# Optimization experiments

Hardware: AMD Instinct MI355X
Metric: run time of the kernel (lower is better)

Reference implementation:

```python
import jax, jax.numpy as jnp
import numpy as np

B, N, HID = 2, 2048, 1024
NH = 16
HD = HID // NH

def setup_inputs() -> dict:
    key = jax.random.key(0)
    ks = jax.random.split(key, 5)
    s = 0.02
    return {
        "hidden_states": jax.random.normal(ks[0], (B, N, HID), jnp.float32),
        "attention_mask": jnp.zeros((B, 1, 1, N), jnp.float32),
        "Wq": jax.random.normal(ks[1], (HID, HID), jnp.float32) * s,
        "bq": jnp.zeros((HID,), jnp.float32),
        "Wk": jax.random.normal(ks[2], (HID, HID), jnp.float32) * s,
        "bk": jnp.zeros((HID,), jnp.float32),
        "Wv": jax.random.normal(ks[3], (HID, HID), jnp.float32) * s,
        "bv": jnp.zeros((HID,), jnp.float32),
    }

def reference(hidden_states, attention_mask, Wq, bq, Wk, bk, Wv, bv):
    b, n, _ = hidden_states.shape
    def split_heads(t):  # [b,n,hid] -> [b,h,n,d]
        return t.reshape(b, n, NH, HD).transpose(0, 2, 1, 3)
    q = split_heads(hidden_states @ Wq.T + bq)
    k = split_heads(hidden_states @ Wk.T + bk)
    v = split_heads(hidden_states @ Wv.T + bv)
    scores = jnp.einsum('bhnd,bhmd->bhnm', q, k) / jnp.sqrt(jnp.float32(HD)).astype(q.dtype)
    scores = scores + attention_mask
    scores = jnp.maximum(scores, jnp.finfo(scores.dtype).min)
    probs = jax.nn.softmax(scores, axis=-1)
    out = jnp.einsum('bhnm,bhmd->bhnd', probs, v)
    return out.transpose(0, 2, 1, 3).reshape(b, n, NH * HD)
```

## Files before the change

### kernel.cpp

```cpp
#include <hip/hip_runtime.h>

typedef unsigned short u16;
typedef unsigned int   u32;
typedef __attribute__((ext_vector_type(8))) short bf16x8;
typedef __attribute__((ext_vector_type(4))) float f32x4;
typedef __attribute__((ext_vector_type(2))) unsigned int u32x2;

__device__ __forceinline__ float bf2f(u16 u) { return __uint_as_float(((u32)u) << 16); }
__device__ __forceinline__ u16 f2bf(float f) {
    return (u16)((__float_as_uint(f) + 0x8000u) >> 16);
}
__device__ __forceinline__ void gload16(const void* g, void* l) {
    __builtin_amdgcn_global_load_lds((const __attribute__((address_space(1))) void*)g,
                                     (__attribute__((address_space(3))) void*)l, 16, 0, 0);
}

struct us4 { u16 x, y, z, w; };
__global__ void cvt_all(const float* __restrict__ hs, const float* __restrict__ wq,
                        const float* __restrict__ wk, const float* __restrict__ wv,
                        u16* __restrict__ dst)
{
    int i = blockIdx.x * blockDim.x + threadIdx.x;
    const int stride = gridDim.x * blockDim.x;
    us4* d4 = (us4*)dst;
    for (; i < 1835008; i += stride) {
        const float4* s4;
        int j = i;
        if (j < 1048576)      { s4 = (const float4*)hs; }
        else if (j < 1310720) { s4 = (const float4*)wq; j -= 1048576; }
        else if (j < 1572864) { s4 = (const float4*)wk; j -= 1310720; }
        else                  { s4 = (const float4*)wv; j -= 1572864; }
        float4 v = s4[j];
        us4 o;
        o.x = f2bf(v.x); o.y = f2bf(v.y); o.z = f2bf(v.z); o.w = f2bf(v.w);
        d4[i] = o;
    }
}

__global__ __launch_bounds__(256) void qkv_gemm(
    const u16* __restrict__ hs,
    const u16* __restrict__ Wq, const u16* __restrict__ Wk, const u16* __restrict__ Wv,
    const float* __restrict__ bq, const float* __restrict__ bk, const float* __restrict__ bv,
    u16* __restrict__ oq, u16* __restrict__ ok, u16* __restrict__ ovt)
{
    __shared__ u16 smem[12288];
    u16* sA = smem;
    u16* sB = smem + 4096;

    const int tid  = threadIdx.x;
    const int lane = tid & 63;
    const int wv_  = tid >> 6;
    const int c15  = lane & 15;
    const int q4   = lane >> 4;
    const int rb   = blockIdx.x;
    const int mat  = blockIdx.y >> 3;
    const int cb   = blockIdx.y & 7;

    const u16*   W    = (mat == 0) ? Wq : (mat == 1 ? Wk : Wv);
    const float* bias = (mat == 0) ? bq : (mat == 1 ? bk : bv);

    f32x4 acc[4][2] = {};

    int rA[2], cA[2], rB[4], cB[4];
#pragma unroll
    for (int p = 0; p < 2; ++p) {
        const int ch = p * 256 + tid;
        rA[p] = ch >> 3; cA[p] = ((ch & 7) ^ (rA[p] & 7)) * 8;
    }
#pragma unroll
    for (int p = 0; p < 4; ++p) {
        const int ch = p * 256 + tid;
        rB[p] = ch >> 3; cB[p] = ((ch & 7) ^ (rB[p] & 7)) * 8;
    }
    const u16* gA = hs + (rb * 64) * 1024;
    const u16* gB = W + (cb * 128) * 1024;
    const int swz = c15 & 7;

    for (int kb = 0; kb < 1024; kb += 64) {
        __syncthreads();
#pragma unroll
        for (int p = 0; p < 2; ++p)
            gload16(gA + rA[p] * 1024 + kb + cA[p], sA + (p * 256 + wv_ * 64) * 8);
#pragma unroll
        for (int p = 0; p < 4; ++p)
            gload16(gB + rB[p] * 1024 + kb + cB[p], sB + (p * 256 + wv_ * 64) * 8);
        __syncthreads();

#pragma unroll
        for (int kk = 0; kk < 2; ++kk) {
            const int cpos = ((kk * 4 + q4) ^ swz) * 8;
            bf16x8 af[4], bf[2];
#pragma unroll
            for (int mt = 0; mt < 4; ++mt)
                af[mt] = *(const bf16x8*)(sA + (mt * 16 + c15) * 64 + cpos);
#pragma unroll
            for (int nt = 0; nt < 2; ++nt)
                bf[nt] = *(const bf16x8*)(sB + (wv_ * 32 + nt * 16 + c15) * 64 + cpos);
#pragma unroll
            for (int mt = 0; mt < 4; ++mt)
#pragma unroll
                for (int nt = 0; nt < 2; ++nt)
                    acc[mt][nt] = __builtin_amdgcn_mfma_f32_16x16x32_bf16(
                        af[mt], bf[nt], acc[mt][nt], 0, 0, 0);
        }
    }

    __syncthreads();
    const int hcol = cb * 2 + (wv_ >> 1);
    const int dbase = (wv_ & 1) * 32;
    float bvv[2];
#pragma unroll
    for (int nt = 0; nt < 2; ++nt)
        bvv[nt] = bias[cb * 128 + wv_ * 32 + nt * 16 + c15];

    u16* sc = smem + wv_ * 2560;
    if (mat != 2) {
        u16* dst = (mat == 0) ? oq : ok;
#pragma unroll
        for (int mt = 0; mt < 4; ++mt)
#pragma unroll
            for (int nt = 0; nt < 2; ++nt)
#pragma unroll
                for (int r = 0; r < 4; ++r)
                    sc[(mt * 16 + q4 * 4 + r) * 40 + nt * 16 + c15] =
                        f2bf(acc[mt][nt][r] + bvv[nt]);
#pragma unroll
        for (int i = 0; i < 4; ++i) {
            const int rl = i * 16 + (lane >> 2);
            const int c0 = (lane & 3) * 8;
            bf16x8 vv = *(const bf16x8*)(sc + rl * 40 + c0);
            const int n = rb * 64 + rl;
            const int bb = n >> 11, nn = n & 2047;
            *(bf16x8*)(dst + (((bb * 16 + hcol) * 2048) + nn) * 64 + dbase + c0) = vv;
        }
    } else {
#pragma unroll
        for (int mt = 0; mt < 4; ++mt)
#pragma unroll
            for (int nt = 0; nt < 2; ++nt)
#pragma unroll
                for (int r = 0; r < 4; ++r)
                    sc[(nt * 16 + c15) * 72 + mt * 16 + q4 * 4 + r] =
                        f2bf(acc[mt][nt][r] + bvv[nt]);
#pragma unroll
        for (int i = 0; i < 4; ++i) {
            const int dp = i * 8 + (lane >> 3);
            const int nl = (lane & 7) * 8;
            bf16x8 vv = *(const bf16x8*)(sc + dp * 72 + nl);
            const int n = rb * 64 + nl;
            const int bb = n >> 11, nn = n & 2047;
            *(bf16x8*)(ovt + (((bb * 16 + hcol) * 64) + dbase + dp) * 2048 + nn) = vv;
        }
    }
}

__global__ __launch_bounds__(256) void attn(
    const u16* __restrict__ qm, const u16* __restrict__ km, const u16* __restrict__ vtm,
    const float* __restrict__ mask, float* __restrict__ out)
{
    __shared__ u16 sK[64 * 64];
    __shared__ u16 sVT[64 * 64];

    const int tid = threadIdx.x, lane = tid & 63, w = tid >> 6;
    const int c15 = lane & 15, q4 = lane >> 4;
    const int qt = blockIdx.x;
    const int bh = blockIdx.y;
    const int b = bh >> 4;

    bf16x8 qf[2][2];
    const u16* qbase = qm + (bh * 2048 + qt * 128 + w * 32) * 64;
#pragma unroll
    for (int rt = 0; rt < 2; ++rt)
#pragma unroll
        for (int kt = 0; kt < 2; ++kt)
            qf[rt][kt] = *(const bf16x8*)(qbase + (rt * 16 + c15) * 64 + kt * 32 + q4 * 8);

    float l_acc[2] = {0.f, 0.f};
    f32x4 accO[2][4] = {};

    const u16* kbase  = km  + bh * 2048 * 64;
    const u16* vtbase = vtm + bh * 64 * 2048;

    const int r0 = tid >> 3,         cc0 = ((tid & 7) ^ (r0 & 7)) * 8;
    const int r1 = (256 + tid) >> 3, cc1 = ((tid & 7) ^ (r1 & 7)) * 8;

    for (int it = 0; it < 32; ++it) {
        const int kb = it * 64;
        __syncthreads();

        gload16(kbase + (kb + r0) * 64 + cc0, sK + (w * 64) * 8);
        gload16(kbase + (kb + r1) * 64 + cc1, sK + (256 + w * 64) * 8);
        gload16(vtbase + r0 * 2048 + kb + cc0, sVT + (w * 64) * 8);
        gload16(vtbase + r1 * 2048 + kb + cc1, sVT + (256 + w * 64) * 8);
        __syncthreads();

        float mkv[4][4];
#pragma unroll
        for (int ktile = 0; ktile < 4; ++ktile) {
            float4 m4 = *(const float4*)(mask + b * 2048 + kb + ktile * 16 + q4 * 4);
            mkv[ktile][0] = m4.x; mkv[ktile][1] = m4.y;
            mkv[ktile][2] = m4.z; mkv[ktile][3] = m4.w;
        }

        f32x4 accST[4][2] = {};
#pragma unroll
        for (int kt = 0; kt < 2; ++kt) {
            bf16x8 kf[4];
#pragma unroll
            for (int ktile = 0; ktile < 4; ++ktile) {
                const int key = ktile * 16 + c15;
                const int cpos = (kt * 4 + q4) ^ (key & 7);
                kf[ktile] = *(const bf16x8*)(sK + key * 64 + cpos * 8);
            }
#pragma unroll
            for (int ktile = 0; ktile < 4; ++ktile)
#pragma unroll
                for (int rt = 0; rt < 2; ++rt)
                    accST[ktile][rt] = __builtin_amdgcn_mfma_f32_16x16x32_bf16(
                        kf[ktile], qf[rt][kt], accST[ktile][rt], 0, 0, 0);
        }

        u32 pu[4][2][2];
#pragma unroll
        for (int ktile = 0; ktile < 4; ++ktile)
#pragma unroll
            for (int rt = 0; rt < 2; ++rt) {
                u32 a[4];
#pragma unroll
                for (int r = 0; r < 4; ++r) {
                    const float p = __expf(fmaf(accST[ktile][rt][r], 0.125f, mkv[ktile][r]));
                    l_acc[rt] += p;
                    a[r] = __float_as_uint(p) + 0x8000u;
                }
                pu[ktile][rt][0] = (a[0] >> 16) | (a[1] & 0xFFFF0000u);
                pu[ktile][rt][1] = (a[2] >> 16) | (a[3] & 0xFFFF0000u);
            }

#pragma unroll
        for (int g = 0; g < 2; ++g) {
            bf16x8 pA[2];
#pragma unroll
            for (int rt = 0; rt < 2; ++rt) {
                union { bf16x8 v; u32 u[4]; } t;
                t.u[0] = pu[2 * g][rt][0];
                t.u[1] = pu[2 * g][rt][1];
                t.u[2] = pu[2 * g + 1][rt][0];
                t.u[3] = pu[2 * g + 1][rt][1];
                pA[rt] = t.v;
            }
            bf16x8 vB[4];
#pragma unroll
            for (int nt = 0; nt < 4; ++nt) {
                const int d = nt * 16 + c15;
                const int pc0 = (4 * g + (q4 >> 1)) ^ (d & 7);
                const int pc1 = (4 * g + 2 + (q4 >> 1)) ^ (d & 7);
                u32x2 v0 = *(const u32x2*)(sVT + d * 64 + pc0 * 8 + (q4 & 1) * 4);
                u32x2 v1 = *(const u32x2*)(sVT + d * 64 + pc1 * 8 + (q4 & 1) * 4);
                union { bf16x8 v; u32 u[4]; } t;
                t.u[0] = v0.x; t.u[1] = v0.y; t.u[2] = v1.x; t.u[3] = v1.y;
                vB[nt] = t.v;
            }
#pragma unroll
            for (int rt = 0; rt < 2; ++rt)
#pragma unroll
                for (int nt = 0; nt < 4; ++nt)
                    accO[rt][nt] = __builtin_amdgcn_mfma_f32_16x16x32_bf16(
                        pA[rt], vB[nt], accO[rt][nt], 0, 0, 0);
        }
    }

#pragma unroll
    for (int rt = 0; rt < 2; ++rt) {
        l_acc[rt] += __shfl_xor(l_acc[rt], 16);
        l_acc[rt] += __shfl_xor(l_acc[rt], 32);
    }

    const int h = bh & 15;
#pragma unroll
    for (int rt = 0; rt < 2; ++rt) {
        float inv[4];
#pragma unroll
        for (int r = 0; r < 4; ++r)
            inv[r] = 1.0f / __shfl(l_acc[rt], q4 * 4 + r);
#pragma unroll
        for (int nt = 0; nt < 4; ++nt)
#pragma unroll
            for (int r = 0; r < 4; ++r) {
                const int qrow = qt * 128 + w * 32 + rt * 16 + q4 * 4 + r;
                const int d = nt * 16 + c15;
                out[(b * 2048 + qrow) * 1024 + h * 64 + d] = accO[rt][nt][r] * inv[r];
            }
    }
}

extern "C" void kernel_launch(void* const* d_in, const int* in_sizes, int n_in,
                              void* d_out, int out_size, void* d_ws, size_t ws_size,
                              hipStream_t stream)
{
    const float* hs   = (const float*)d_in[0];
    const float* mask = (const float*)d_in[1];
    const float* Wq   = (const float*)d_in[2];
    const float* bq   = (const float*)d_in[3];
    const float* Wk   = (const float*)d_in[4];
    const float* bk   = (const float*)d_in[5];
    const float* Wv   = (const float*)d_in[6];
    const float* bv   = (const float*)d_in[7];

    u16* ws   = (u16*)d_ws;
    u16* qw   = ws;
    u16* kw   = ws + 4194304;
    u16* vtw  = ws + 8388608;
    u16* hsb  = ws + 12582912;
    u16* wqb  = ws + 16777216;
    u16* wkb  = ws + 17825792;
    u16* wvb  = ws + 18874368;

    cvt_all<<<1024, 256, 0, stream>>>(hs, Wq, Wk, Wv, hsb);

    qkv_gemm<<<dim3(64, 24), 256, 0, stream>>>(hsb, wqb, wkb, wvb, bq, bk, bv, qw, kw, vtw);
    attn<<<dim3(16, 32), 256, 0, stream>>>(qw, kw, vtw, mask, (float*)d_out);
}
```

Baseline: 183.1 us.

## Split attention block into 8 waves of 16 query rows with permuted K layout

The attention kernel now launches 512 threads per block, with each of 8 waves handling 16 query rows instead of 32. Because each thread issues one K and one V global-to-LDS load per iteration, the K rows are stored in a permuted order, so the P fragment lines up with full 16-byte V^T reads instead of paired 8-byte reads. The kernel also folds log2(e) into the scale and mask to use exp2, and uses the hardware packed bf16 convert. The aim is more waves in flight to hide latency and fewer LDS and ALU instructions, at the cost of reloading each K/V tile into LDS for only half as much MFMA work per wave.

After: 179.3 us. 1.02x faster.

```diff
diff --git a/kernel.cpp b/kernel.cpp
--- a/kernel.cpp
+++ b/kernel.cpp
@@ -9,6 +9,11 @@
 __device__ __forceinline__ float bf2f(u16 u) { return __uint_as_float(((u32)u) << 16); }
 __device__ __forceinline__ u16 f2bf(float f) {
     return (u16)((__float_as_uint(f) + 0x8000u) >> 16);
+}
+__device__ __forceinline__ u32 cvt_pk_bf16(float lo, float hi) {
+    u32 r;
+    asm("v_cvt_pk_bf16_f32 %0, %1, %2" : "=v"(r) : "v"(lo), "v"(hi));
+    return r;
 }
 __device__ __forceinline__ void gload16(const void* g, void* l) {
     __builtin_amdgcn_global_load_lds((const __attribute__((address_space(1))) void*)g,
@@ -154,7 +159,7 @@
     }
 }
 
-__global__ __launch_bounds__(256) void attn(
+__global__ __launch_bounds__(512, 4) void attn(
     const u16* __restrict__ qm, const u16* __restrict__ km, const u16* __restrict__ vtm,
     const float* __restrict__ mask, float* __restrict__ out)
 {
@@ -167,130 +172,114 @@
     const int bh = blockIdx.y;
     const int b = bh >> 4;
 
-    bf16x8 qf[2][2];
-    const u16* qbase = qm + (bh * 2048 + qt * 128 + w * 32) * 64;
-#pragma unroll
-    for (int rt = 0; rt < 2; ++rt)
-#pragma unroll
-        for (int kt = 0; kt < 2; ++kt)
-            qf[rt][kt] = *(const bf16x8*)(qbase + (rt * 16 + c15) * 64 + kt * 32 + q4 * 8);
-
-    float l_acc[2] = {0.f, 0.f};
-    f32x4 accO[2][4] = {};
+    bf16x8 qf[2];
+    const u16* qbase = qm + (bh * 2048 + qt * 128 + w * 16) * 64;
+#pragma unroll
+    for (int kt = 0; kt < 2; ++kt)
+        qf[kt] = *(const bf16x8*)(qbase + c15 * 64 + kt * 32 + q4 * 8);
+
+    float l_acc = 0.f;
+    f32x4 accO[4] = {};
 
     const u16* kbase  = km  + bh * 2048 * 64;
     const u16* vtbase = vtm + bh * 64 * 2048;
 
-    const int r0 = tid >> 3,         cc0 = ((tid & 7) ^ (r0 & 7)) * 8;
-    const int r1 = (256 + tid) >> 3, cc1 = ((tid & 7) ^ (r1 & 7)) * 8;
+    const int r  = tid >> 3;
+    const int cc = tid & 7;
+    const int col = (cc ^ (r & 7)) * 8;
+    const int pr  = (r & 0x23) | ((r & 0x0C) << 1) | ((r & 0x10) >> 2);
+    const int offK = pr * 64 + col;
+    const int offV = r * 2048 + col;
+    u16* dstK = sK  + w * 512;
+    u16* dstV = sVT + w * 512;
+
+    const float* mbase = mask + b * 2048 + 8 * q4;
 
     for (int it = 0; it < 32; ++it) {
         const int kb = it * 64;
         __syncthreads();
 
-        gload16(kbase + (kb + r0) * 64 + cc0, sK + (w * 64) * 8);
-        gload16(kbase + (kb + r1) * 64 + cc1, sK + (256 + w * 64) * 8);
-        gload16(vtbase + r0 * 2048 + kb + cc0, sVT + (w * 64) * 8);
-        gload16(vtbase + r1 * 2048 + kb + cc1, sVT + (256 + w * 64) * 8);
+        gload16(kbase + kb * 64 + offK, dstK);
+        gload16(vtbase + kb + offV, dstV);
         __syncthreads();
 
         float mkv[4][4];
 #pragma unroll
-        for (int ktile = 0; ktile < 4; ++ktile) {
-            float4 m4 = *(const float4*)(mask + b * 2048 + kb + ktile * 16 + q4 * 4);
-            mkv[ktile][0] = m4.x; mkv[ktile][1] = m4.y;
-            mkv[ktile][2] = m4.z; mkv[ktile][3] = m4.w;
-        }
-
-        f32x4 accST[4][2] = {};
+        for (int t = 0; t < 4; ++t) {
+            float4 m4 = *(const float4*)(mbase + kb + 32 * (t >> 1) + 4 * (t & 1));
+            mkv[t][0] = m4.x * 1.4426950408889634f;
+            mkv[t][1] = m4.y * 1.4426950408889634f;
+            mkv[t][2] = m4.z * 1.4426950408889634f;
+            mkv[t][3] = m4.w * 1.4426950408889634f;
+        }
+
+        f32x4 accST[4] = {};
 #pragma unroll
         for (int kt = 0; kt < 2; ++kt) {
             bf16x8 kf[4];
 #pragma unroll
-            for (int ktile = 0; ktile < 4; ++ktile) {
-                const int key = ktile * 16 + c15;
-                const int cpos = (kt * 4 + q4) ^ (key & 7);
-                kf[ktile] = *(const bf16x8*)(sK + key * 64 + cpos * 8);
+            for (int t = 0; t < 4; ++t) {
+                const int rho = t * 16 + c15;
+                const int cpos = (kt * 4 + q4) ^ (rho & 7);
+                kf[t] = *(const bf16x8*)(sK + rho * 64 + cpos * 8);
             }
 #pragma unroll
-            for (int ktile = 0; ktile < 4; ++ktile)
-#pragma unroll
-                for (int rt = 0; rt < 2; ++rt)
-                    accST[ktile][rt] = __builtin_amdgcn_mfma_f32_16x16x32_bf16(
-                        kf[ktile], qf[rt][kt], accST[ktile][rt], 0, 0, 0);
-        }
-
-        u32 pu[4][2][2];
-#pragma unroll
-        for (int ktile = 0; ktile < 4; ++ktile)
-#pragma unroll
-            for (int rt = 0; rt < 2; ++rt) {
-                u32 a[4];
-#pragma unroll
-                for (int r = 0; r < 4; ++r) {
-                    const float p = __expf(fmaf(accST[ktile][rt][r], 0.125f, mkv[ktile][r]));
-                    l_acc[rt] += p;
-                    a[r] = __float_as_uint(p) + 0x8000u;
-                }
-                pu[ktile][rt][0] = (a[0] >> 16) | (a[1] & 0xFFFF0000u);
-                pu[ktile][rt][1] = (a[2] >> 16) | (a[3] & 0xFFFF0000u);
+            for (int t = 0; t < 4; ++t)
+                accST[t] = __builtin_amdgcn_mfma_f32_16x16x32_bf16(
+                    kf[t], qf[kt], accST[t], 0, 0, 0);
+        }
+
+        u32 pu[4][2];
+#pragma unroll
+        for (int t = 0; t < 4; ++t) {
+            float p[4];
+#pragma unroll
+            for (int rr = 0; rr < 4; ++rr) {
+                p[rr] = __builtin_amdgcn_exp2f(
+                    fmaf(accST[t][rr], 0.18033688011112042f, mkv[t][rr]));
+                l_acc += p[rr];
             }
+            pu[t][0] = cvt_pk_bf16(p[0], p[1]);
+            pu[t][1] = cvt_pk_bf16(p[2], p[3]);
+        }
 
 #pragma unroll
         for (int g = 0; g < 2; ++g) {
-            bf16x8 pA[2];
-#pragma unroll
-            for (int rt = 0; rt < 2; ++rt) {
-                union { bf16x8 v; u32 u[4]; } t;
-                t.u[0] = pu[2 * g][rt][0];
-                t.u[1] = pu[2 * g][rt][1];
-                t.u[2] = pu[2 * g + 1][rt][0];
-                t.u[3] = pu[2 * g + 1][rt][1];
-                pA[rt] = t.v;
-            }
+            union { bf16x8 v; u32 u[4]; } ta;
+            ta.u[0] = pu[2 * g][0];
+            ta.u[1] = pu[2 * g][1];
+            ta.u[2] = pu[2 * g + 1][0];
+            ta.u[3] = pu[2 * g + 1][1];
             bf16x8 vB[4];
 #pragma unroll
             for (int nt = 0; nt < 4; ++nt) {
                 const int d = nt * 16 + c15;
-                const int pc0 = (4 * g + (q4 >> 1)) ^ (d & 7);
-                const int pc1 = (4 * g + 2 + (q4 >> 1)) ^ (d & 7);
-                u32x2 v0 = *(const u32x2*)(sVT + d * 64 + pc0 * 8 + (q4 & 1) * 4);
-                u32x2 v1 = *(const u32x2*)(sVT + d * 64 + pc1 * 8 + (q4 & 1) * 4);
-                union { bf16x8 v; u32 u[4]; } t;
-                t.u[0] = v0.x; t.u[1] = v0.y; t.u[2] = v1.x; t.u[3] = v1.y;
-                vB[nt] = t.v;
+                const int pc = (4 * g + q4) ^ (d & 7);
+                vB[nt] = *(const bf16x8*)(sVT + d * 64 + pc * 8);
             }
 #pragma unroll
-            for (int rt = 0; rt < 2; ++rt)
-#pragma unroll
-                for (int nt = 0; nt < 4; ++nt)
-                    accO[rt][nt] = __builtin_amdgcn_mfma_f32_16x16x32_bf16(
-                        pA[rt], vB[nt], accO[rt][nt], 0, 0, 0);
-        }
-    }
-
-#pragma unroll
-    for (int rt = 0; rt < 2; ++rt) {
-        l_acc[rt] += __shfl_xor(l_acc[rt], 16);
-        l_acc[rt] += __shfl_xor(l_acc[rt], 32);
-    }
+            for (int nt = 0; nt < 4; ++nt)
+                accO[nt] = __builtin_amdgcn_mfma_f32_16x16x32_bf16(
+                    ta.v, vB[nt], accO[nt], 0, 0, 0);
+        }
+    }
+
+    l_acc += __shfl_xor(l_acc, 16);
+    l_acc += __shfl_xor(l_acc, 32);
 
     const int h = bh & 15;
-#pragma unroll
-    for (int rt = 0; rt < 2; ++rt) {
-        float inv[4];
-#pragma unroll
-        for (int r = 0; r < 4; ++r)
-            inv[r] = 1.0f / __shfl(l_acc[rt], q4 * 4 + r);
-#pragma unroll
-        for (int nt = 0; nt < 4; ++nt)
-#pragma unroll
-            for (int r = 0; r < 4; ++r) {
-                const int qrow = qt * 128 + w * 32 + rt * 16 + q4 * 4 + r;
-                const int d = nt * 16 + c15;
-                out[(b * 2048 + qrow) * 1024 + h * 64 + d] = accO[rt][nt][r] * inv[r];
-            }
-    }
+    float inv[4];
+#pragma unroll
+    for (int rr = 0; rr < 4; ++rr)
+        inv[rr] = 1.0f / __shfl(l_acc, q4 * 4 + rr);
+#pragma unroll
+    for (int nt = 0; nt < 4; ++nt)
+#pragma unroll
+        for (int rr = 0; rr < 4; ++rr) {
+            const int qrow = qt * 128 + w * 16 + q4 * 4 + rr;
+            const int d = nt * 16 + c15;
+            out[(b * 2048 + qrow) * 1024 + h * 64 + d] = accO[nt][rr] * inv[rr];
+        }
 }
 
 extern "C" void kernel_launch(void* const* d_in, const int* in_sizes, int n_in,
@@ -318,5 +307,5 @@
     cvt_all<<<1024, 256, 0, stream>>>(hs, Wq, Wk, Wv, hsb);
 
     qkv_gemm<<<dim3(64, 24), 256, 0, stream>>>(hsb, wqb, wkb, wvb, bq, bk, bv, qw, kw, vtw);
-    attn<<<dim3(16, 32), 256, 0, stream>>>(qw, kw, vtw, mask, (float*)d_out);
-}
+    attn<<<dim3(16, 32), 512, 0, stream>>>(qw, kw, vtw, mask, (float*)d_out);
+}
```
